# Kernel optimization log

Hardware: AMD Instinct MI355X
Metric: run time of the kernel (lower is better)

The kernel has to match this reference:

```python
import jax, jax.numpy as jnp
import numpy as np

DIM_X, H1, H2 = 1024, 2048, 512
SL, SU = 8192, 16384
K_TRIES = 8  # vectorized stand-in for the per-sample rejection-sampling while-loop


def setup_inputs() -> dict:
    key = jax.random.key(0)
    ks = jax.random.split(key, 10)
    s = 0.02
    return {
        "X_l": jax.random.normal(ks[0], (SL, DIM_X), jnp.float32),
        "y_l": jax.random.normal(ks[1], (SL,), jnp.float32),
        "X_u": jax.random.normal(ks[2], (SU, DIM_X), jnp.float32),
        "y_u": jax.random.normal(ks[3], (SU,), jnp.float32),
        "W1": jax.random.normal(ks[4], (DIM_X, H1), jnp.float32) * s,
        "b1": jnp.zeros((H1,), jnp.float32),
        "W2": jax.random.normal(ks[5], (H1, H2), jnp.float32) * s,
        "b2": jnp.zeros((H2,), jnp.float32),
        "W3": jax.random.normal(ks[6], (H2, 1), jnp.float32) * s,
        "b3": jnp.zeros((1,), jnp.float32),
    }


def _sample_pairs(key, y_l, size_u):
    """For each unlabeled sample, draw a labeled pair (a, b) with a != b and
    y_l[a] != y_l[b] (mirrors torch.randperm + rejection loop). K candidate
    draws per sample; first valid candidate is taken (valid w.h.p. for
    continuous y_l)."""
    size_l = y_l.shape[0]
    ka, kb = jax.random.split(key)
    ia = jax.random.randint(ka, (size_u, K_TRIES), 0, size_l)  # [SU, K]
    ib = jax.random.randint(kb, (size_u, K_TRIES), 0, size_l)
    valid = (ia != ib) & (y_l[ia] != y_l[ib])
    first = jnp.argmax(valid, axis=1)  # first valid candidate per row
    a = jnp.take_along_axis(ia, first[:, None], axis=1)[:, 0]
    b = jnp.take_along_axis(ib, first[:, None], axis=1)[:, 0]
    return a, b


def reference(X_l, y_l, X_u, y_u, W1, b1, W2, b2, W3, b3):
    def encode(x):
        h = jax.nn.relu(x @ W1 + b1)
        return jax.nn.relu(h @ W2 + b2)

    feat_l = encode(X_l)          # [SL, H2]
    feat_u = encode(X_u)          # [SU, H2]
    y_hat = feat_l @ W3 + b3      # [SL, 1]

    a, b = _sample_pairs(jax.random.key(42), y_l, X_u.shape[0])
    k = (y_u - y_l[b]) / (y_l[a] - y_l[b])            # [SU]
    feat_comb = k[:, None] * feat_l[a] + (1.0 - k)[:, None] * feat_l[b]
    return feat_u, feat_comb, y_hat
```

## Files before the change

kernel.cpp:

```cpp
#include <hip/hip_runtime.h>
#include <stdint.h>

#define SLAB 8192
#define SUNL 16384
#define DIMX 1024
#define HID1 2048
#define HID2 512
#define KTRIES 8
#define MTOT (SLAB + SUNL)

typedef __attribute__((ext_vector_type(8))) short bf16x8;
typedef __attribute__((ext_vector_type(4))) float f32x4;

__device__ __forceinline__ unsigned short f2bf(float f) {
  union { float f; uint32_t u; } c; c.f = f;
  return (unsigned short)((c.u + 0x7fffu + ((c.u >> 16) & 1u)) >> 16);
}

__device__ __forceinline__ void async16(const void* g, void* l) {
  __builtin_amdgcn_global_load_lds(
      (const __attribute__((address_space(1))) unsigned int*)g,
      (__attribute__((address_space(3))) unsigned int*)l,
      16, 0, 0);
}

struct U2 { uint32_t x, y; };

__device__ __forceinline__ U2 threefry(uint32_t k0, uint32_t k1, uint32_t x0, uint32_t x1) {
  uint32_t ks2 = k0 ^ k1 ^ 0x1BD11BDAu;
  x0 += k0; x1 += k1;
#define TF_R(r) { x0 += x1; x1 = (x1 << (r)) | (x1 >> (32 - (r))); x1 ^= x0; }
  TF_R(13) TF_R(15) TF_R(26) TF_R(6)
  x0 += k1; x1 += ks2 + 1u;
  TF_R(17) TF_R(29) TF_R(16) TF_R(24)
  x0 += ks2; x1 += k0 + 2u;
  TF_R(13) TF_R(15) TF_R(26) TF_R(6)
  x0 += k0; x1 += k1 + 3u;
  TF_R(17) TF_R(29) TF_R(16) TF_R(24)
  x0 += k1; x1 += ks2 + 4u;
  TF_R(13) TF_R(15) TF_R(26) TF_R(6)
  x0 += ks2; x1 += k0 + 5u;
#undef TF_R
  return {x0, x1};
}

#define XL_BLOCKS (SLAB * DIMX / 4 / 256)
#define CAST_BLOCKS (MTOT * DIMX / 4 / 256)
#define T1_NBX (HID1 / 32)
#define T1_BLOCKS ((HID1 / 32) * (DIMX / 32))
#define T2_NBX (HID2 / 32)
#define T2_BLOCKS ((HID2 / 32) * (HID1 / 32))
#define PAIR_BLOCKS (SUNL / 256)
#define PREP_BLOCKS (CAST_BLOCKS + T1_BLOCKS + T2_BLOCKS + PAIR_BLOCKS)

__global__ __launch_bounds__(256) void prep_kernel(
    const float* __restrict__ Xl, const float* __restrict__ Xu,
    const float* __restrict__ W1, const float* __restrict__ W2,
    const float* __restrict__ y_l, const float* __restrict__ y_u,
    unsigned short* __restrict__ X_bf, unsigned short* __restrict__ W1T,
    unsigned short* __restrict__ W2T,
    int* __restrict__ ia, int* __restrict__ ib, float* __restrict__ kv)
{
  __shared__ float t[32][33];
  int b = blockIdx.x;
  int tid = threadIdx.x;

  if (b < CAST_BLOCKS) {
    const float* src; size_t i, doff;
    if (b < XL_BLOCKS) { src = Xl; i = (size_t)b * 256 + tid; doff = 0; }
    else { src = Xu; i = (size_t)(b - XL_BLOCKS) * 256 + tid; doff = (size_t)SLAB * DIMX / 4; }
    float4 v = ((const float4*)src)[i];
    ushort4 o;
    o.x = f2bf(v.x); o.y = f2bf(v.y); o.z = f2bf(v.z); o.w = f2bf(v.w);
    ((ushort4*)X_bf)[doff + i] = o;
  } else if (b < CAST_BLOCKS + T1_BLOCKS + T2_BLOCKS) {
    const float* W; unsigned short* WT; int K, N, bx, by;
    if (b < CAST_BLOCKS + T1_BLOCKS) {
      int tb = b - CAST_BLOCKS;
      W = W1; WT = W1T; K = DIMX; N = HID1; bx = tb % T1_NBX; by = tb / T1_NBX;
    } else {
      int tb = b - CAST_BLOCKS - T1_BLOCKS;
      W = W2; WT = W2T; K = HID1; N = HID2; bx = tb % T2_NBX; by = tb / T2_NBX;
    }
    int k0 = by * 32, n0 = bx * 32;
    int tx = tid & 31, ty = tid >> 5;
#pragma unroll
    for (int i = 0; i < 32; i += 8)
      t[ty + i][tx] = W[(size_t)(k0 + ty + i) * N + n0 + tx];
    __syncthreads();
#pragma unroll
    for (int i = 0; i < 32; i += 8)
      WT[(size_t)(n0 + ty + i) * K + k0 + tx] = f2bf(t[tx][ty + i]);
  } else {
    int r = (b - CAST_BLOCKS - T1_BLOCKS - T2_BLOCKS) * 256 + tid;
    U2 ka  = threefry(0u, 42u, 0u, 0u);
    U2 kb  = threefry(0u, 42u, 0u, 1u);
    U2 k2a = threefry(ka.x, ka.y, 0u, 1u);
    U2 k2b = threefry(kb.x, kb.y, 0u, 1u);
    int iav[KTRIES], ibv[KTRIES];
#pragma unroll
    for (int c = 0; c < KTRIES; ++c) {
      uint32_t tt = (uint32_t)(r * KTRIES + c);
      U2 oa = threefry(k2a.x, k2a.y, 0u, tt);
      U2 ob = threefry(k2b.x, k2b.y, 0u, tt);
      iav[c] = (int)((oa.x ^ oa.y) & (SLAB - 1));
      ibv[c] = (int)((ob.x ^ ob.y) & (SLAB - 1));
    }
    int a = iav[0], bb2 = ibv[0];
#pragma unroll
    for (int c = 0; c < KTRIES; ++c) {
      if (iav[c] != ibv[c] && y_l[iav[c]] != y_l[ibv[c]]) { a = iav[c]; bb2 = ibv[c]; break; }
    }
    float ya = y_l[a], yb = y_l[bb2];
    ia[r] = a; ib[r] = bb2; kv[r] = (y_u[r] - yb) / (ya - yb);
  }
}

#define GROUP_M 8
#define MFMA_B16(a, b, c) __builtin_amdgcn_mfma_f32_16x16x32_bf16(a, b, c, 0, 0, 0)

template<bool S1, bool S2, int VMC>
__device__ __forceinline__ void ktile256(
    unsigned short* Ac, unsigned short* Bc, unsigned short* Ao,
    const unsigned short* gA, const unsigned short* gB,
    int K, int k1, int k2, int ldst,
    int abase, int bbase, int sw0, int sw1,
    f32x4 (&acc)[8][4])
{
  bf16x8 a0[4][2], a1[4][2], b0[2][2], b1[2][2];

  if (S1) {
    async16(gA + (size_t)64 * K + k1,  Ao + 4096 + ldst);
    async16(gA + (size_t)192 * K + k1, Ao + 12288 + ldst);
  }

#pragma unroll
  for (int i = 0; i < 4; ++i) {
    a0[i][0] = *(const bf16x8*)(Ac + abase + i * 1024 + sw0);
    a0[i][1] = *(const bf16x8*)(Ac + abase + i * 1024 + sw1);
  }
#pragma unroll
  for (int j = 0; j < 2; ++j) {
    b0[j][0] = *(const bf16x8*)(Bc + bbase + j * 1024 + sw0);
    b0[j][1] = *(const bf16x8*)(Bc + bbase + j * 1024 + sw1);
  }
  __builtin_amdgcn_sched_barrier(0);
#pragma unroll
  for (int j = 0; j < 2; ++j) {
    b1[j][0] = *(const bf16x8*)(Bc + bbase + (j + 2) * 1024 + sw0);
    b1[j][1] = *(const bf16x8*)(Bc + bbase + (j + 2) * 1024 + sw1);
  }
  __builtin_amdgcn_sched_barrier(0);
#pragma unroll
  for (int i = 0; i < 4; ++i) {
    a1[i][0] = *(const bf16x8*)(Ac + abase + (i + 4) * 1024 + sw0);
    a1[i][1] = *(const bf16x8*)(Ac + abase + (i + 4) * 1024 + sw1);
  }
  __builtin_amdgcn_sched_barrier(0);

  asm volatile("s_waitcnt lgkmcnt(12)" ::: "memory");
  __builtin_amdgcn_sched_barrier(0);
  __builtin_amdgcn_s_setprio(1);
#pragma unroll
  for (int i = 0; i < 4; ++i)
#pragma unroll
    for (int j = 0; j < 2; ++j) {
      acc[i][j] = MFMA_B16(a0[i][0], b0[j][0], acc[i][j]);
      acc[i][j] = MFMA_B16(a0[i][1], b0[j][1], acc[i][j]);
    }
  __builtin_amdgcn_s_setprio(0);
  __builtin_amdgcn_s_barrier();

  if (S2) {
    async16(gA + k2,                   Ac + ldst);
    async16(gA + (size_t)128 * K + k2, Ac + 8192 + ldst);
  }
  asm volatile("s_waitcnt lgkmcnt(8)" ::: "memory");
  __builtin_amdgcn_sched_barrier(0);
  __builtin_amdgcn_s_setprio(1);
#pragma unroll
  for (int i = 0; i < 4; ++i)
#pragma unroll
    for (int j = 0; j < 2; ++j) {
      acc[i][j + 2] = MFMA_B16(a0[i][0], b1[j][0], acc[i][j + 2]);
      acc[i][j + 2] = MFMA_B16(a0[i][1], b1[j][1], acc[i][j + 2]);
    }
  __builtin_amdgcn_s_setprio(0);
  __builtin_amdgcn_s_barrier();

  if (S2) {
    async16(gB + k2,                  Bc + ldst);
    async16(gB + (size_t)64 * K + k2, Bc + 4096 + ldst);
  }
  asm volatile("s_waitcnt lgkmcnt(0)" ::: "memory");
  __builtin_amdgcn_sched_barrier(0);
  __builtin_amdgcn_s_setprio(1);
#pragma unroll
  for (int i = 0; i < 4; ++i)
#pragma unroll
    for (int j = 0; j < 2; ++j) {
      acc[i + 4][j] = MFMA_B16(a1[i][0], b0[j][0], acc[i + 4][j]);
      acc[i + 4][j] = MFMA_B16(a1[i][1], b0[j][1], acc[i + 4][j]);
    }
  __builtin_amdgcn_s_setprio(0);
  __builtin_amdgcn_s_barrier();

  if (S2) {
    async16(gB + (size_t)128 * K + k2, Bc + 8192 + ldst);
    async16(gB + (size_t)192 * K + k2, Bc + 12288 + ldst);
  }
  __builtin_amdgcn_s_setprio(1);
#pragma unroll
  for (int i = 0; i < 4; ++i)
#pragma unroll
    for (int j = 0; j < 2; ++j) {
      acc[i + 4][j + 2] = MFMA_B16(a1[i][0], b1[j][0], acc[i + 4][j + 2]);
      acc[i + 4][j + 2] = MFMA_B16(a1[i][1], b1[j][1], acc[i + 4][j + 2]);
    }
  __builtin_amdgcn_s_setprio(0);
  if (VMC == 6)      asm volatile("s_waitcnt vmcnt(6)" ::: "memory");
  else if (VMC == 0) asm volatile("s_waitcnt vmcnt(0)" ::: "memory");
  __builtin_amdgcn_s_barrier();
}

template<int OUT_BF16, int RELU>
__global__ __launch_bounds__(512, 2) void gemm_bt_256(
    const unsigned short* __restrict__ A,
    const unsigned short* __restrict__ Bt,
    const float* __restrict__ bias,
    void* __restrict__ C0, void* __restrict__ C1, int Msplit,
    int M, int N, int K)
{
  __shared__ unsigned short As[2][16384];
  __shared__ unsigned short Bs[2][16384];

  const int tid  = threadIdx.x;
  const int wave = tid >> 6;
  const int lane = tid & 63;

  const int nbx = N >> 8;
  const int gsize = nbx * GROUP_M;
  const int grp = blockIdx.x / gsize, within = blockIdx.x % gsize;
  const int m0 = (grp * GROUP_M + (within % GROUP_M)) << 8;
  const int n0 = (within / GROUP_M) << 8;

  const int wm = (wave >> 2) << 7;
  const int wn = (wave & 3) << 6;

  const int srow   = tid >> 3;
  const int schunk = (tid & 7) ^ (srow & 7);
  const unsigned short* gA = A  + (size_t)(m0 + srow) * K + schunk * 8;
  const unsigned short* gB = Bt + (size_t)(n0 + srow) * K + schunk * 8;
  const int ldst = wave << 9;

  const int fr = lane & 15, q = lane >> 4;
  const int sw0 = (q << 3) ^ ((fr & 7) << 3);
  const int sw1 = sw0 ^ 32;
  const int abase = (wm + fr) << 6;
  const int bbase = (wn + fr) << 6;

  f32x4 acc[8][4] = {};

  unsigned short* A0p = &As[0][0]; unsigned short* B0p = &Bs[0][0];
  unsigned short* A1p = &As[1][0]; unsigned short* B1p = &Bs[1][0];

  async16(gA,                        A0p + ldst);
  async16(gA + (size_t)64 * K,       A0p + 4096 + ldst);
  async16(gA + (size_t)128 * K,      A0p + 8192 + ldst);
  async16(gA + (size_t)192 * K,      A0p + 12288 + ldst);
  async16(gB,                        B0p + ldst);
  async16(gB + (size_t)64 * K,       B0p + 4096 + ldst);
  async16(gB + (size_t)128 * K,      B0p + 8192 + ldst);
  async16(gB + (size_t)192 * K,      B0p + 12288 + ldst);
  async16(gA + 64,                   A1p + ldst);
  async16(gA + (size_t)128 * K + 64, A1p + 8192 + ldst);
  async16(gB + 64,                   B1p + ldst);
  async16(gB + (size_t)64 * K + 64,  B1p + 4096 + ldst);
  async16(gB + (size_t)128 * K + 64, B1p + 8192 + ldst);
  async16(gB + (size_t)192 * K + 64, B1p + 12288 + ldst);
  asm volatile("s_waitcnt vmcnt(6)" ::: "memory");
  __builtin_amdgcn_s_barrier();

  const int NT = K >> 6;
#pragma unroll 1
  for (int t = 0; t < NT - 2; ++t) {
    const int bb = t & 1;
    ktile256<true, true, 6>(&As[bb][0], &Bs[bb][0], &As[bb ^ 1][0],
                            gA, gB, K, (t + 1) << 6, (t + 2) << 6,
                            ldst, abase, bbase, sw0, sw1, acc);
  }
  {
    const int bb = (NT - 2) & 1;
    ktile256<true, false, 0>(&As[bb][0], &Bs[bb][0], &As[bb ^ 1][0],
                             gA, gB, K, (NT - 1) << 6, 0,
                             ldst, abase, bbase, sw0, sw1, acc);
  }
  {
    const int bb = (NT - 1) & 1;
    ktile256<false, false, -1>(&As[bb][0], &Bs[bb][0], &As[bb ^ 1][0],
                               gA, gB, K, 0, 0,
                               ldst, abase, bbase, sw0, sw1, acc);
  }

  void* Cb = (m0 < Msplit) ? C0 : C1;
  const int mbase = (m0 < Msplit) ? m0 : (m0 - Msplit);
  const int crow = mbase + wm + (lane >> 4) * 4;
  const int ccol = n0 + wn + (lane & 15);
  float bv[4];
#pragma unroll
  for (int j = 0; j < 4; ++j) bv[j] = bias[ccol + j * 16];
#pragma unroll
  for (int i = 0; i < 8; ++i) {
#pragma unroll
    for (int r = 0; r < 4; ++r) {
      size_t base = (size_t)(crow + i * 16 + r) * N + ccol;
#pragma unroll
      for (int j = 0; j < 4; ++j) {
        float v = acc[i][j][r] + bv[j];
        if (RELU) v = fmaxf(v, 0.0f);
        if (OUT_BF16) ((unsigned short*)Cb)[base + j * 16] = f2bf(v);
        else          ((float*)Cb)[base + j * 16] = v;
      }
    }
  }
}

#define COMB_BLOCKS (SUNL / 2)
#define YHAT_BLOCKS (SLAB / 4)
#define POST_BLOCKS (COMB_BLOCKS + YHAT_BLOCKS)

__global__ __launch_bounds__(256) void post_kernel(
    const float* __restrict__ feat_l, const float* __restrict__ W3,
    const float* __restrict__ b3, const int* __restrict__ ia,
    const int* __restrict__ ib, const float* __restrict__ kv,
    float* __restrict__ out_comb, float* __restrict__ out_yhat)
{
  int b = blockIdx.x;
  if (b < COMB_BLOCKS) {
    int row = b * 2 + (threadIdx.x >> 7);
    int c = (threadIdx.x & 127) << 2;
    float k = kv[row];
    float km1 = 1.0f - k;
    float4 fa = *(const float4*)(feat_l + (size_t)ia[row] * HID2 + c);
    float4 fb = *(const float4*)(feat_l + (size_t)ib[row] * HID2 + c);
    float4 o;
    o.x = k * fa.x + km1 * fb.x;
    o.y = k * fa.y + km1 * fb.y;
    o.z = k * fa.z + km1 * fb.z;
    o.w = k * fa.w + km1 * fb.w;
    *(float4*)(out_comb + (size_t)row * HID2 + c) = o;
  } else {
    int wave = threadIdx.x >> 6;
    int lane = threadIdx.x & 63;
    int row = (b - COMB_BLOCKS) * 4 + wave;
    const float* f = feat_l + (size_t)row * HID2;
    float s = 0.f;
#pragma unroll
    for (int j = 0; j < HID2 / 64; ++j) s = fmaf(f[lane + j * 64], W3[lane + j * 64], s);
#pragma unroll
    for (int off = 32; off; off >>= 1) s += __shfl_down(s, off);
    if (lane == 0) out_yhat[row] = s + b3[0];
  }
}

extern "C" void kernel_launch(void* const* d_in, const int* in_sizes, int n_in,
                              void* d_out, int out_size, void* d_ws, size_t ws_size,
                              hipStream_t stream)
{
  const float* X_l = (const float*)d_in[0];
  const float* y_l = (const float*)d_in[1];
  const float* X_u = (const float*)d_in[2];
  const float* y_u = (const float*)d_in[3];
  const float* W1  = (const float*)d_in[4];
  const float* b1  = (const float*)d_in[5];
  const float* W2  = (const float*)d_in[6];
  const float* b2  = (const float*)d_in[7];
  const float* W3  = (const float*)d_in[8];
  const float* b3  = (const float*)d_in[9];

  float* out_featu = (float*)d_out;
  float* out_comb  = out_featu + (size_t)SUNL * HID2;
  float* out_yhat  = out_comb + (size_t)SUNL * HID2;

  unsigned short* X_bf  = (unsigned short*)d_ws;
  unsigned short* W1T   = X_bf + (size_t)MTOT * DIMX;
  unsigned short* W2T   = W1T + (size_t)HID1 * DIMX;
  unsigned short* H_bf  = W2T + (size_t)HID2 * HID1;
  float* feat_l = (float*)(H_bf + (size_t)MTOT * HID1);
  int*   ai = (int*)(feat_l + (size_t)SLAB * HID2);
  int*   bi = ai + SUNL;
  float* kv = (float*)(bi + SUNL);

  prep_kernel<<<dim3(PREP_BLOCKS), dim3(256), 0, stream>>>(
      X_l, X_u, W1, W2, y_l, y_u, X_bf, W1T, W2T, ai, bi, kv);

  gemm_bt_256<1, 1><<<dim3((HID1 / 256) * (MTOT / 256)), dim3(512), 0, stream>>>(
      X_bf, W1T, b1, H_bf, H_bf, MTOT , MTOT, HID1, DIMX);

  gemm_bt_256<0, 1><<<dim3((HID2 / 256) * (MTOT / 256)), dim3(512), 0, stream>>>(
      H_bf, W2T, b2, feat_l, out_featu, SLAB, MTOT, HID2, HID1);

  post_kernel<<<dim3(POST_BLOCKS), dim3(256), 0, stream>>>(
      feat_l, W3, b3, ai, bi, kv, out_comb, out_yhat);
}
```

Before: 344.9 us.

## Software-pipeline GEMM k-loop by deferring a1-block MFMAs into next tile

Restructures the GEMM k-tile loop so the last two MFMA quadrants (a1×b0, a1×b1) of each tile run at the start of the next tile, interleaved with the LDS fragment reads for that tile. Register fragments are double-buffered across two FragSet structures, the loop is unrolled by two with an explicit prologue and epilogue, and barriers per tile drop from four to two, with all B refills issued together. The aim is to hide LDS read latency behind MFMA work and cut synchronization, at the cost of higher register pressure with two fragment sets live under launch_bounds(512,2), which could cause spills.

```diff
diff --git a/kernel.cpp b/kernel.cpp
--- a/kernel.cpp
+++ b/kernel.cpp
@@ -118,109 +118,114 @@
 
 #define GROUP_M 8
 #define MFMA_B16(a, b, c) __builtin_amdgcn_mfma_f32_16x16x32_bf16(a, b, c, 0, 0, 0)
-
-template<bool S1, bool S2, int VMC>
-__device__ __forceinline__ void ktile256(
+#define SBAR __builtin_amdgcn_sched_barrier(0)
+
+struct FragSet { bf16x8 a0[4][2], a1[4][2], b0[2][2], b1[2][2]; };
+
+template<bool M2P, bool M1, bool S1F, bool S2F, int VMC, bool BARS>
+__device__ __forceinline__ void ktile(
+    FragSet& nf, FragSet& of,
     unsigned short* Ac, unsigned short* Bc, unsigned short* Ao,
     const unsigned short* gA, const unsigned short* gB,
     int K, int k1, int k2, int ldst,
     int abase, int bbase, int sw0, int sw1,
     f32x4 (&acc)[8][4])
 {
-  bf16x8 a0[4][2], a1[4][2], b0[2][2], b1[2][2];
-
-  if (S1) {
+  if (M1) {
+#pragma unroll
+    for (int i = 0; i < 4; ++i) {
+      nf.a0[i][0] = *(const bf16x8*)(Ac + abase + i * 1024 + sw0);
+      nf.a0[i][1] = *(const bf16x8*)(Ac + abase + i * 1024 + sw1);
+    }
+    SBAR;
+  }
+  if (S1F) {
     async16(gA + (size_t)64 * K + k1,  Ao + 4096 + ldst);
     async16(gA + (size_t)192 * K + k1, Ao + 12288 + ldst);
-  }
-
-#pragma unroll
-  for (int i = 0; i < 4; ++i) {
-    a0[i][0] = *(const bf16x8*)(Ac + abase + i * 1024 + sw0);
-    a0[i][1] = *(const bf16x8*)(Ac + abase + i * 1024 + sw1);
-  }
-#pragma unroll
-  for (int j = 0; j < 2; ++j) {
-    b0[j][0] = *(const bf16x8*)(Bc + bbase + j * 1024 + sw0);
-    b0[j][1] = *(const bf16x8*)(Bc + bbase + j * 1024 + sw1);
-  }
-  __builtin_amdgcn_sched_barrier(0);
-#pragma unroll
-  for (int j = 0; j < 2; ++j) {
-    b1[j][0] = *(const bf16x8*)(Bc + bbase + (j + 2) * 1024 + sw0);
-    b1[j][1] = *(const bf16x8*)(Bc + bbase + (j + 2) * 1024 + sw1);
-  }
-  __builtin_amdgcn_sched_barrier(0);
-#pragma unroll
-  for (int i = 0; i < 4; ++i) {
-    a1[i][0] = *(const bf16x8*)(Ac + abase + (i + 4) * 1024 + sw0);
-    a1[i][1] = *(const bf16x8*)(Ac + abase + (i + 4) * 1024 + sw1);
-  }
-  __builtin_amdgcn_sched_barrier(0);
-
-  asm volatile("s_waitcnt lgkmcnt(12)" ::: "memory");
-  __builtin_amdgcn_sched_barrier(0);
-  __builtin_amdgcn_s_setprio(1);
-#pragma unroll
-  for (int i = 0; i < 4; ++i)
+    SBAR;
+  }
+  if (M2P) {
+    __builtin_amdgcn_s_setprio(1);
+#pragma unroll
+    for (int i = 0; i < 4; ++i)
+#pragma unroll
+      for (int j = 0; j < 2; ++j) {
+        acc[i + 4][j] = MFMA_B16(of.a1[i][0], of.b0[j][0], acc[i + 4][j]);
+        acc[i + 4][j] = MFMA_B16(of.a1[i][1], of.b0[j][1], acc[i + 4][j]);
+      }
+    __builtin_amdgcn_s_setprio(0);
+    SBAR;
+  }
+  if (M1) {
 #pragma unroll
     for (int j = 0; j < 2; ++j) {
-      acc[i][j] = MFMA_B16(a0[i][0], b0[j][0], acc[i][j]);
-      acc[i][j] = MFMA_B16(a0[i][1], b0[j][1], acc[i][j]);
-    }
-  __builtin_amdgcn_s_setprio(0);
-  __builtin_amdgcn_s_barrier();
-
-  if (S2) {
+      nf.b0[j][0] = *(const bf16x8*)(Bc + bbase + j * 1024 + sw0);
+      nf.b0[j][1] = *(const bf16x8*)(Bc + bbase + j * 1024 + sw1);
+    }
+    SBAR;
+  }
+  if (M2P) {
+    __builtin_amdgcn_s_setprio(1);
+#pragma unroll
+    for (int i = 0; i < 4; ++i)
+#pragma unroll
+      for (int j = 0; j < 2; ++j) {
+        acc[i + 4][j + 2] = MFMA_B16(of.a1[i][0], of.b1[j][0], acc[i + 4][j + 2]);
+        acc[i + 4][j + 2] = MFMA_B16(of.a1[i][1], of.b1[j][1], acc[i + 4][j + 2]);
+      }
+    __builtin_amdgcn_s_setprio(0);
+    SBAR;
+  }
+  if (M1) {
+#pragma unroll
+    for (int j = 0; j < 2; ++j) {
+      nf.b1[j][0] = *(const bf16x8*)(Bc + bbase + (j + 2) * 1024 + sw0);
+      nf.b1[j][1] = *(const bf16x8*)(Bc + bbase + (j + 2) * 1024 + sw1);
+    }
+#pragma unroll
+    for (int i = 0; i < 4; ++i) {
+      nf.a1[i][0] = *(const bf16x8*)(Ac + abase + (i + 4) * 1024 + sw0);
+      nf.a1[i][1] = *(const bf16x8*)(Ac + abase + (i + 4) * 1024 + sw1);
+    }
+    SBAR;
+    asm volatile("s_waitcnt lgkmcnt(12)" ::: "memory");
+    SBAR;
+    __builtin_amdgcn_s_setprio(1);
+#pragma unroll
+    for (int i = 0; i < 4; ++i)
+#pragma unroll
+      for (int j = 0; j < 2; ++j) {
+        acc[i][j] = MFMA_B16(nf.a0[i][0], nf.b0[j][0], acc[i][j]);
+        acc[i][j] = MFMA_B16(nf.a0[i][1], nf.b0[j][1], acc[i][j]);
+      }
+    __builtin_amdgcn_s_setprio(0);
+    asm volatile("s_waitcnt lgkmcnt(8)" ::: "memory");
+    SBAR;
+    __builtin_amdgcn_s_setprio(1);
+#pragma unroll
+    for (int i = 0; i < 4; ++i)
+#pragma unroll
+      for (int j = 0; j < 2; ++j) {
+        acc[i][j + 2] = MFMA_B16(nf.a0[i][0], nf.b1[j][0], acc[i][j + 2]);
+        acc[i][j + 2] = MFMA_B16(nf.a0[i][1], nf.b1[j][1], acc[i][j + 2]);
+      }
+    __builtin_amdgcn_s_setprio(0);
+    asm volatile("s_waitcnt lgkmcnt(0)" ::: "memory");
+    SBAR;
+  }
+  if (BARS) __builtin_amdgcn_s_barrier();
+  if (S2F) {
     async16(gA + k2,                   Ac + ldst);
     async16(gA + (size_t)128 * K + k2, Ac + 8192 + ldst);
-  }
-  asm volatile("s_waitcnt lgkmcnt(8)" ::: "memory");
-  __builtin_amdgcn_sched_barrier(0);
-  __builtin_amdgcn_s_setprio(1);
-#pragma unroll
-  for (int i = 0; i < 4; ++i)
-#pragma unroll
-    for (int j = 0; j < 2; ++j) {
-      acc[i][j + 2] = MFMA_B16(a0[i][0], b1[j][0], acc[i][j + 2]);
-      acc[i][j + 2] = MFMA_B16(a0[i][1], b1[j][1], acc[i][j + 2]);
-    }
-  __builtin_amdgcn_s_setprio(0);
-  __builtin_amdgcn_s_barrier();
-
-  if (S2) {
-    async16(gB + k2,                  Bc + ldst);
-    async16(gB + (size_t)64 * K + k2, Bc + 4096 + ldst);
-  }
-  asm volatile("s_waitcnt lgkmcnt(0)" ::: "memory");
-  __builtin_amdgcn_sched_barrier(0);
-  __builtin_amdgcn_s_setprio(1);
-#pragma unroll
-  for (int i = 0; i < 4; ++i)
-#pragma unroll
-    for (int j = 0; j < 2; ++j) {
-      acc[i + 4][j] = MFMA_B16(a1[i][0], b0[j][0], acc[i + 4][j]);
-      acc[i + 4][j] = MFMA_B16(a1[i][1], b0[j][1], acc[i + 4][j]);
-    }
-  __builtin_amdgcn_s_setprio(0);
-  __builtin_amdgcn_s_barrier();
-
-  if (S2) {
+    async16(gB + k2,                   Bc + ldst);
+    async16(gB + (size_t)64 * K + k2,  Bc + 4096 + ldst);
     async16(gB + (size_t)128 * K + k2, Bc + 8192 + ldst);
     async16(gB + (size_t)192 * K + k2, Bc + 12288 + ldst);
-  }
-  __builtin_amdgcn_s_setprio(1);
-#pragma unroll
-  for (int i = 0; i < 4; ++i)
-#pragma unroll
-    for (int j = 0; j < 2; ++j) {
-      acc[i + 4][j + 2] = MFMA_B16(a1[i][0], b1[j][0], acc[i + 4][j + 2]);
-      acc[i + 4][j + 2] = MFMA_B16(a1[i][1], b1[j][1], acc[i + 4][j + 2]);
-    }
-  __builtin_amdgcn_s_setprio(0);
+    SBAR;
+  }
   if (VMC == 6)      asm volatile("s_waitcnt vmcnt(6)" ::: "memory");
   else if (VMC == 0) asm volatile("s_waitcnt vmcnt(0)" ::: "memory");
-  __builtin_amdgcn_s_barrier();
+  if (BARS) __builtin_amdgcn_s_barrier();
 }
 
 template<int OUT_BF16, int RELU>
@@ -260,6 +265,7 @@
   const int bbase = (wn + fr) << 6;
 
   f32x4 acc[8][4] = {};
+  FragSet fE, fO;
 
   unsigned short* A0p = &As[0][0]; unsigned short* B0p = &Bs[0][0];
   unsigned short* A1p = &As[1][0]; unsigned short* B1p = &Bs[1][0];
@@ -282,25 +288,25 @@
   __builtin_amdgcn_s_barrier();
 
   const int NT = K >> 6;
+
+  ktile<false, true, true, true, 6, true>(fE, fE, A0p, B0p, A1p, gA, gB, K,
+      64, 128, ldst, abase, bbase, sw0, sw1, acc);
+
 #pragma unroll 1
-  for (int t = 0; t < NT - 2; ++t) {
-    const int bb = t & 1;
-    ktile256<true, true, 6>(&As[bb][0], &Bs[bb][0], &As[bb ^ 1][0],
-                            gA, gB, K, (t + 1) << 6, (t + 2) << 6,
-                            ldst, abase, bbase, sw0, sw1, acc);
-  }
-  {
-    const int bb = (NT - 2) & 1;
-    ktile256<true, false, 0>(&As[bb][0], &Bs[bb][0], &As[bb ^ 1][0],
-                             gA, gB, K, (NT - 1) << 6, 0,
-                             ldst, abase, bbase, sw0, sw1, acc);
-  }
-  {
-    const int bb = (NT - 1) & 1;
-    ktile256<false, false, -1>(&As[bb][0], &Bs[bb][0], &As[bb ^ 1][0],
-                               gA, gB, K, 0, 0,
-                               ldst, abase, bbase, sw0, sw1, acc);
-  }
+  for (int t = 1; t <= NT - 5; t += 2) {
+    ktile<true, true, true, true, 6, true>(fO, fE, A1p, B1p, A0p, gA, gB, K,
+        (t + 1) << 6, (t + 2) << 6, ldst, abase, bbase, sw0, sw1, acc);
+    ktile<true, true, true, true, 6, true>(fE, fO, A0p, B0p, A1p, gA, gB, K,
+        (t + 2) << 6, (t + 3) << 6, ldst, abase, bbase, sw0, sw1, acc);
+  }
+  ktile<true, true, true, true, 6, true>(fO, fE, A1p, B1p, A0p, gA, gB, K,
+      (NT - 2) << 6, (NT - 1) << 6, ldst, abase, bbase, sw0, sw1, acc);
+  ktile<true, true, true, false, 0, true>(fE, fO, A0p, B0p, A1p, gA, gB, K,
+      (NT - 1) << 6, 0, ldst, abase, bbase, sw0, sw1, acc);
+  ktile<true, true, false, false, -1, false>(fO, fE, A1p, B1p, A0p, gA, gB, K,
+      0, 0, ldst, abase, bbase, sw0, sw1, acc);
+  ktile<true, false, false, false, -1, false>(fE, fO, A1p, B1p, A0p, gA, gB, K,
+      0, 0, ldst, abase, bbase, sw0, sw1, acc);
 
   void* Cb = (m0 < Msplit) ? C0 : C1;
   const int mbase = (m0 < Msplit) ? m0 : (m0 - Msplit);
```

Result: slower. 643.1 us (+86.5%).
